# Performance work log

Measured on AMD Instinct MI355X. Metric: run time of the kernel, lower is better.

The kernel has to match this reference:

```python
import jax, jax.numpy as jnp
import numpy as np
from jax import lax

DN = ('NHWC', 'HWIO', 'NHWC')

def _conv(x, k, b, stride=1):
    return lax.conv_general_dilated(x, k, (stride, stride), 'SAME', dimension_numbers=DN) + b

def _tconv(x, k, b):
    return lax.conv_transpose(x, k, (2, 2), 'SAME', dimension_numbers=DN) + b


def setup_inputs() -> dict:
    key = jax.random.key(0)
    ks = jax.random.split(key, 32)
    ki = iter(ks)
    def w(shape, scale=0.05):
        return (jax.random.normal(next(ki), shape, dtype=jnp.float32) * scale)
    inp = {}
    inp['x'] = jax.random.uniform(next(ki), (8, 128, 128, 3), dtype=jnp.float32)
    # encoder
    inp['k1'],  inp['b1']  = w((11, 11, 3, 32)),   jnp.zeros((32,), jnp.float32)
    inp['k1c'], inp['b1c'] = w((3, 3, 32, 32)),    jnp.zeros((32,), jnp.float32)
    inp['k2'],  inp['b2']  = w((11, 11, 32, 64)),  jnp.zeros((64,), jnp.float32)
    inp['k2c'], inp['b2c'] = w((3, 3, 64, 64)),    jnp.zeros((64,), jnp.float32)
    inp['k3'],  inp['b3']  = w((11, 11, 64, 128)), jnp.zeros((128,), jnp.float32)
    inp['k3c'], inp['b3c'] = w((3, 3, 128, 128)),  jnp.zeros((128,), jnp.float32)
    # codebook (codebookSize=256, latent dim 128)
    inp['codebook'] = w((256, 128), 0.1)
    # decoder
    inp['tk1'],  inp['tb1']  = w((5, 5, 128, 64)), jnp.zeros((64,), jnp.float32)
    inp['tk1c'], inp['tb1c'] = w((3, 3, 64, 64)),  jnp.zeros((64,), jnp.float32)
    inp['tk2'],  inp['tb2']  = w((5, 5, 64, 32)),  jnp.zeros((32,), jnp.float32)
    inp['tk2c'], inp['tb2c'] = w((3, 3, 32, 32)),  jnp.zeros((32,), jnp.float32)
    inp['tk3'],  inp['tb3']  = w((5, 5, 32, 32)),  jnp.zeros((32,), jnp.float32)
    inp['tk3c'], inp['tb3c'] = w((3, 3, 32, 3)),   jnp.zeros((3,), jnp.float32)
    return inp


def reference(x, k1, b1, k1c, b1c, k2, b2, k2c, b2c, k3, b3, k3c, b3c,
              codebook, tk1, tb1, tk1c, tb1c, tk2, tb2, tk2c, tb2c,
              tk3, tb3, tk3c, tb3c):
    act = jax.nn.silu  # flax.nnx.swish
    # encoder
    d1 = act(_conv(x, k1, b1, 2))
    d1 = act(_conv(d1, k1c, b1c, 1))
    d2 = act(_conv(d1, k2, b2, 2))
    d2 = act(_conv(d2, k2c, b2c, 1))
    d3 = act(_conv(d2, k3, b3, 2))
    d3 = _conv(d3, k3c, b3c, 1)               # [B, H/8, W/8, 128]
    # vector quantization: squared L2 to each codebook entry
    lat = d3.reshape(-1, 1, 128)              # [N, 1, 128]
    eu_dis = jnp.sum((lat - codebook[None]) ** 2, axis=-1)   # [N, 256]
    idx = jnp.argmin(eu_dis, axis=-1)         # [N]
    quantized = jnp.take(codebook, idx, axis=0).reshape(d3.shape)
    # straight-through estimator
    replaced = lax.stop_gradient(quantized - d3) + d3
    # decoder
    d4 = act(_tconv(replaced, tk1, tb1))
    d4 = act(_conv(d4, tk1c, tb1c, 1))
    d5 = act(_tconv(d4, tk2, tb2))
    d5 = act(_conv(d5, tk2c, tb2c, 1))
    d6 = act(_tconv(d5, tk3, tb3))
    out = _conv(d6, tk3c, tb3c, 1)            # [B, H, W, 3]
    return out
```

## Files before the change

kernel.cpp:

```cpp
#include <hip/hip_runtime.h>

#define DI __device__ __forceinline__
DI float silu_f(float x){ return x * (1.0f/(1.0f+__expf(-x))); }

template<int X> struct LOG2 { static constexpr int v = 1 + LOG2<X/2>::v; };
template<> struct LOG2<1> { static constexpr int v = 0; };

template<int KH,int KW,int STRIDE,int PAD,int CIN,int COUT,int NPIX,
         bool ACT,bool BIAS,int G,int CS,int TOW>
__global__ __launch_bounds__(256) void conv_k(
    const float* __restrict__ in, const float* __restrict__ w,
    const float* __restrict__ bias, float* __restrict__ out,
    int N,int H,int W,int OH,int OW)
{
  constexpr int CLEN = CIN/G;
  constexpr int COB  = COUT/CS;
  constexpr int COQ  = COB/4;
  constexpr int GSH  = LOG2<G>::v;
  constexpr int CSH  = LOG2<CS>::v;
  constexpr int TAPF = CLEN*COB;
  constexpr bool SALL = (KH*KW*TAPF*4) <= 47*1024;
  constexpr int NTAP = SALL ? KH*KW : KW;
  static_assert(CLEN==3 || (CLEN%4)==0, "ci");
  __shared__ float sw[NTAP*TAPF];
  constexpr int SPAN = (TOW>0) ? (TOW-1)*STRIDE + KW : 1;
  constexpr int ROWS = (TOW>0) ? ((256/COQ)*NPIX)/TOW : 1;
  constexpr int CQ4  = (TOW>0 && CLEN!=3) ? CLEN/4 : 1;
  constexpr int SI_F = (TOW==0) ? 1 : (CLEN==3 ? ROWS*SPAN*3 : ROWS*CQ4*SPAN*4);
  __shared__ float si[SI_F];
  static_assert(TOW==0 || NPIX<=2, "tow npix");
  static_assert(TOW==0 || ((256/COQ)*NPIX) % TOW == 0, "rows");

  const int g  = blockIdx.x & (G-1);
  const int cs = (blockIdx.x >> GSH) & (CS-1);
  const int bx = blockIdx.x >> (GSH+CSH);
  const int total = N*OH*OW;
  if (G>1) out += (size_t)g * total * COUT;
  const int ci_off  = g*CLEN;
  const int co_base = cs*COB;

  int idx = bx*256 + (int)threadIdx.x;
  int cq = idx % COQ;
  int pg = idx / COQ;
  int co = cq*4;
  int gco = co_base + co;
  int p0 = pg*NPIX;

  float acc[NPIX][4] = {};
  int iy0[NPIX], ix0[NPIX]; const float* base[NPIX]; bool pv[NPIX];
#pragma unroll
  for (int t=0;t<NPIX;t++){
    int p=p0+t; pv[t]=(p<total); int pp=pv[t]?p:0;
    int ox=pp%OW; int r=pp/OW; int oy=r%OH; int n=r/OH;
    iy0[t]=oy*STRIDE-PAD; ix0[t]=ox*STRIDE-PAD;
    base[t]=in+(size_t)n*H*W*CIN + ci_off;
  }

  auto stage = [&](int tap0){
    constexpr int TQ = TAPF/4;
    constexpr int V  = NTAP*TQ;
    for (int v=threadIdx.x; v<V; v+=256){
      int tap = v / TQ; int rem = v - tap*TQ;
      float4 q;
      if constexpr (CS==1){
        const float4* src = (const float4*)(w + ((size_t)(tap0+tap)*CIN + ci_off)*COUT);
        q = src[rem];
      } else if constexpr (CLEN==3){
        int ci = rem / (COB/4); int r2 = rem - ci*(COB/4);
        q = *(const float4*)(w + ((size_t)(tap0+tap)*CIN + ci)*COUT
                               + co_base + r2*4);
      } else {
        int ci = rem / (COB/4); int r2 = rem - ci*(COB/4);
        q = *(const float4*)(w + ((size_t)(tap0+tap)*CIN + ci_off + ci)*COUT
                               + co_base + r2*4);
      }
      *(float4*)(sw + (size_t)tap*TAPF + rem*4) = q;
    }
  };

  if constexpr (SALL){
    stage(0);
    __syncthreads();
  }

  if constexpr (TOW>0){
    const int pb0 = bx * ((256/COQ)*NPIX);
    const int r0  = pb0 / TOW;
    const int oy0 = r0 % OH;
    const int n0  = r0 / OH;
    int myrow[NPIX], oxl[NPIX];
#pragma unroll
    for (int t=0;t<NPIX;t++){
      int pl = p0 + t - pb0;
      myrow[t] = pl / TOW;
      oxl[t]   = pl - myrow[t]*TOW;
    }

    for (int ky=0; ky<KH; ky++){
      __syncthreads();
      if constexpr (!SALL) stage(ky*KW);
      if constexpr (CLEN==3){
        constexpr int INS = ROWS*SPAN;
        for (int v=(int)threadIdx.x; v<INS; v+=256){
          int r  = v / SPAN;
          int ixo= v - r*SPAN;
          int iy = (oy0+r)*STRIDE - PAD + ky;
          int ix = ixo - PAD;
          bool ok = iy>=0 && iy<H && ix>=0 && ix<W;
          const float* ip = in + ((size_t)(n0*H+iy)*W + ix)*CIN;
          si[v*3+0] = ok?ip[0]:0.f;
          si[v*3+1] = ok?ip[1]:0.f;
          si[v*3+2] = ok?ip[2]:0.f;
        }
      } else {
        constexpr int INQ = ROWS*CQ4*SPAN;
        for (int v=(int)threadIdx.x; v<INQ; v+=256){
          int r  = v / (CQ4*SPAN);
          int rm = v - r*(CQ4*SPAN);
          int q  = rm / SPAN;
          int ixo= rm - q*SPAN;
          int iy = (oy0+r)*STRIDE - PAD + ky;
          int ix = ixo - PAD;
          bool ok = iy>=0 && iy<H && ix>=0 && ix<W;
          float4 val = ok ? *(const float4*)(in + ((size_t)(n0*H+iy)*W + ix)*CIN + ci_off + q*4)
                          : make_float4(0.f,0.f,0.f,0.f);
          *(float4*)&si[(size_t)v*4] = val;
        }
      }
      __syncthreads();
      const float* swr = SALL ? sw + (size_t)ky*KW*TAPF : sw;
      for (int kx=0; kx<KW; kx++){
        const float* swt = swr + (size_t)kx*TAPF;
        if constexpr (CLEN==3){
          float wv[3][4];
          *(float4*)wv[0]=*(const float4*)(swt + 0*COB + co);
          *(float4*)wv[1]=*(const float4*)(swt + 1*COB + co);
          *(float4*)wv[2]=*(const float4*)(swt + 2*COB + co);
#pragma unroll
          for (int t=0;t<NPIX;t++){
            const float* sp = &si[(size_t)(myrow[t]*SPAN + oxl[t]*STRIDE + kx)*3];
            float v0=sp[0], v1=sp[1], v2=sp[2];
#pragma unroll
            for (int j=0;j<4;j++)
              acc[t][j]=fmaf(v0,wv[0][j],fmaf(v1,wv[1][j],fmaf(v2,wv[2][j],acc[t][j])));
          }
        } else {
#pragma unroll 2
          for (int c=0; c<CQ4; c++){
            float wv[4][4];
#pragma unroll
            for (int r=0;r<4;r++)
              *(float4*)wv[r] = *(const float4*)(swt + (c*4+r)*COB + co);
#pragma unroll
            for (int t=0;t<NPIX;t++){
              float va[4];
              *(float4*)va = *(const float4*)&si[(size_t)((myrow[t]*CQ4 + c)*SPAN + oxl[t]*STRIDE + kx)*4];
#pragma unroll
              for (int r=0;r<4;r++)
#pragma unroll
                for (int j=0;j<4;j++)
                  acc[t][j]=fmaf(va[r],wv[r][j],acc[t][j]);
            }
          }
        }
      }
    }
  } else {
    for (int ky=0; ky<KH; ky++){
      if constexpr (!SALL){
        __syncthreads();
        stage(ky*KW);
        __syncthreads();
      }
      const float* swr = SALL ? sw + (size_t)ky*KW*TAPF : sw;
      for (int kx=0; kx<KW; kx++){
        const float* swt = swr + (size_t)kx*TAPF;
        const float* ip[NPIX]; bool ok[NPIX];
#pragma unroll
        for (int t=0;t<NPIX;t++){
          int iy=iy0[t]+ky, ix=ix0[t]+kx;
          ok[t]=pv[t] && iy>=0 && iy<H && ix>=0 && ix<W;
          ip[t]=base[t]+(size_t)(iy*W+ix)*CIN;
        }
        if constexpr (CLEN==3){
          float wv[3][4];
          *(float4*)wv[0]=*(const float4*)(swt + 0*COB + co);
          *(float4*)wv[1]=*(const float4*)(swt + 1*COB + co);
          *(float4*)wv[2]=*(const float4*)(swt + 2*COB + co);
#pragma unroll
          for (int t=0;t<NPIX;t++){
            float v0=ok[t]?ip[t][0]:0.f;
            float v1=ok[t]?ip[t][1]:0.f;
            float v2=ok[t]?ip[t][2]:0.f;
#pragma unroll
            for (int j=0;j<4;j++)
              acc[t][j]=fmaf(v0,wv[0][j],fmaf(v1,wv[1][j],fmaf(v2,wv[2][j],acc[t][j])));
          }
        } else {
#pragma unroll 2
          for (int ci=0; ci<CLEN; ci+=4){
            float wv[4][4];
#pragma unroll
            for (int r=0;r<4;r++)
              *(float4*)wv[r] = *(const float4*)(swt + (ci+r)*COB + co);
#pragma unroll
            for (int t=0;t<NPIX;t++){
              float va[4];
              *(float4*)va = ok[t] ? *(const float4*)(ip[t]+ci)
                                   : make_float4(0.f,0.f,0.f,0.f);
#pragma unroll
              for (int r=0;r<4;r++)
#pragma unroll
                for (int j=0;j<4;j++)
                  acc[t][j]=fmaf(va[r],wv[r][j],acc[t][j]);
            }
          }
        }
      }
    }
  }

  float bv[4]={0.f,0.f,0.f,0.f};
  if constexpr (BIAS) *(float4*)bv = *(const float4*)(bias+gco);
#pragma unroll
  for (int t=0;t<NPIX;t++) if (pv[t]){
    float o[4];
#pragma unroll
    for (int j=0;j<4;j++){
      float v = acc[t][j]+bv[j];
      o[j] = ACT ? silu_f(v) : v;
    }
    *(float4*)(out + (size_t)(p0+t)*COUT + gco) = *(float4*)o;
  }
}

template<int G,int COUT,bool ACT>
__global__ __launch_bounds__(256) void reduce_k(
    const float* __restrict__ p, const float* __restrict__ bias,
    float* __restrict__ out, int n)
{
  int i = (blockIdx.x*256+threadIdx.x)*4;
  if (i>=n) return;
  float a[4]; *(float4*)a = *(const float4*)(p+i);
#pragma unroll
  for (int g=1; g<G; g++){
    float b[4]; *(float4*)b = *(const float4*)(p+(size_t)g*n+i);
#pragma unroll
    for (int j=0;j<4;j++) a[j]+=b[j];
  }
  float bv[4]; *(float4*)bv = *(const float4*)(bias + (i % COUT));
#pragma unroll
  for (int j=0;j<4;j++){
    float v=a[j]+bv[j];
    a[j] = ACT ? silu_f(v) : v;
  }
  *(float4*)(out+i) = *(float4*)a;
}

template<int CIN,int COUT,int NPIX,int G,bool DIRECT>
__global__ __launch_bounds__(256) void tconv_k(
    const float* __restrict__ in, const float* __restrict__ w,
    const float* __restrict__ bias, float* __restrict__ out,
    int N,int H,int W,int OH,int OW)
{
  constexpr int COQ  = COUT/4;
  constexpr int CLEN = CIN/G;
  constexpr int GSH  = LOG2<G>::v;
  constexpr int TAPF = CLEN*COUT;
  __shared__ float sw[TAPF];
  const int par = blockIdx.x & 3;
  const int py = par>>1, px = par&1;
  const int g  = (blockIdx.x>>2) & (G-1);
  const int bx = blockIdx.x >> (2+GSH);
  const int NKY = py?3:2, NKX = px?3:2;
  const int OHh=OH>>1, OWh=OW>>1;
  const int total = N*OHh*OWh;
  if (G>1) out += (size_t)g * N*OH*OW*COUT;

  int idx = bx*256 + (int)threadIdx.x;
  int cq = idx % COQ;
  int pg = idx / COQ;
  int co = cq*4;
  int p0 = pg*NPIX;

  float acc[NPIX][4] = {};
  int yy[NPIX], xx[NPIX], nn[NPIX]; const float* base[NPIX]; bool pv[NPIX];
#pragma unroll
  for (int t=0;t<NPIX;t++){
    int p=p0+t; pv[t]=(p<total); int pp=pv[t]?p:0;
    xx[t]=pp%OWh; int r=pp/OWh; yy[t]=r%OHh; nn[t]=r/OHh;
    base[t]=in+(size_t)nn[t]*H*W*CIN + g*CLEN;
  }

  for (int j=0;j<NKY;j++){
    int ky = 2*j + (py?0:1);
    for (int i=0;i<NKX;i++){
      int kx = 2*i + (px?0:1);
      __syncthreads();
      {
        constexpr int V = TAPF/4;
        const float4* src = (const float4*)(w + ((size_t)(ky*5+kx)*CIN + g*CLEN)*COUT);
        for (int v=threadIdx.x; v<V; v+=256) ((float4*)sw)[v]=src[v];
      }
      __syncthreads();
      const float* ip[NPIX]; bool ok[NPIX];
#pragma unroll
      for (int t=0;t<NPIX;t++){
        int iy=yy[t]+j-1, ix=xx[t]+i-1;
        ok[t]=pv[t] && iy>=0 && iy<H && ix>=0 && ix<W;
        ip[t]=base[t]+(size_t)(iy*W+ix)*CIN;
      }
#pragma unroll 2
      for (int ci=0; ci<CLEN; ci+=4){
        float wv[4][4];
#pragma unroll
        for (int r=0;r<4;r++)
          *(float4*)wv[r] = *(const float4*)(sw + (ci+r)*COUT + co);
#pragma unroll
        for (int t=0;t<NPIX;t++){
          float va[4];
          *(float4*)va = ok[t] ? *(const float4*)(ip[t]+ci)
                               : make_float4(0.f,0.f,0.f,0.f);
#pragma unroll
          for (int r=0;r<4;r++)
#pragma unroll
            for (int jj=0;jj<4;jj++)
              acc[t][jj]=fmaf(va[r],wv[r][jj],acc[t][jj]);
        }
      }
    }
  }

  float bv[4]={0.f,0.f,0.f,0.f};
  if constexpr (DIRECT) *(float4*)bv = *(const float4*)(bias+co);
#pragma unroll
  for (int t=0;t<NPIX;t++) if (pv[t]){
    float o[4];
#pragma unroll
    for (int jj=0;jj<4;jj++){
      float v = acc[t][jj]+bv[jj];
      o[jj] = DIRECT ? silu_f(v) : v;
    }
    *(float4*)(out + (((size_t)nn[t]*OH + (2*yy[t]+py))*OW + (2*xx[t]+px))*COUT + co) = *(float4*)o;
  }
}

__global__ __launch_bounds__(256) void vq_k(
    const float* __restrict__ p, const float* __restrict__ bias,
    const float* __restrict__ cb, float* __restrict__ q, int NLat)
{
  __shared__ float slat[4][128];
  int wave = threadIdx.x >> 6;
  int lane = threadIdx.x & 63;
  int l = blockIdx.x*4 + wave;
  if (l >= NLat) return;
  const float* p0 = p + (size_t)l*128;
  const float* p1 = p0 + (size_t)NLat*128;
  slat[wave][lane]    = p0[lane]    + p1[lane]    + bias[lane];
  slat[wave][lane+64] = p0[lane+64] + p1[lane+64] + bias[lane+64];

  float bestd = INFINITY; int besti = 0;
  for (int c0=0;c0<256;c0+=64){
    int c = c0 + lane;
    const float* cp = cb + (size_t)c*128;
    float d = 0.f;
#pragma unroll 8
    for (int k=0;k<128;k+=4){
      float4 cv = *reinterpret_cast<const float4*>(cp+k);
      float d0 = slat[wave][k+0]-cv.x;
      float d1 = slat[wave][k+1]-cv.y;
      float d2 = slat[wave][k+2]-cv.z;
      float d3 = slat[wave][k+3]-cv.w;
      d += d0*d0; d += d1*d1; d += d2*d2; d += d3*d3;
    }
    if (d < bestd) { bestd = d; besti = c; }
  }
  for (int off=32; off; off>>=1){
    float od = __shfl_down(bestd, off);
    int   oi = __shfl_down(besti, off);
    if (od < bestd || (od == bestd && oi < besti)) { bestd=od; besti=oi; }
  }
  besti = __shfl(besti, 0);
  const float* cp = cb + (size_t)besti*128;
  float* qp = q + (size_t)l*128;
  qp[lane]    = cp[lane];
  qp[lane+64] = cp[lane+64];
}

__global__ __launch_bounds__(256) void conv_last_k(
    const float* __restrict__ in, const float* __restrict__ w,
    float* __restrict__ p, int N,int H,int W)
{
  int g = blockIdx.x % 3;
  int bx = blockIdx.x / 3;
  int pix = bx*256 + threadIdx.x;
  int total = N*H*W;
  if (pix>=total) return;
  int x = pix % W; int r = pix / W; int y = r % H; int n = r / H;
  float a0=0.f, a1=0.f, a2=0.f;
  int iy = y + g - 1;
  if (iy>=0 && iy<H){
    const float* base = in + ((size_t)n*H + iy)*W*32;
    for (int kx=0;kx<3;kx++){
      int ix=x+kx-1; if(ix<0||ix>=W) continue;
      const float* ip = base + (size_t)ix*32;
      const float* wp = w + (size_t)((g*3+kx)*32)*3;
#pragma unroll
      for (int ci=0;ci<32;ci+=4){
        float va[4]; *(float4*)va = *(const float4*)(ip+ci);
        float wv[12];
        *(float4*)(wv+0) = *(const float4*)(wp+ci*3+0);
        *(float4*)(wv+4) = *(const float4*)(wp+ci*3+4);
        *(float4*)(wv+8) = *(const float4*)(wp+ci*3+8);
#pragma unroll
        for (int r2=0;r2<4;r2++){
          a0 = fmaf(va[r2], wv[r2*3+0], a0);
          a1 = fmaf(va[r2], wv[r2*3+1], a1);
          a2 = fmaf(va[r2], wv[r2*3+2], a2);
        }
      }
    }
  }
  float* pp = p + (size_t)g*total*3 + (size_t)pix*3;
  pp[0]=a0; pp[1]=a1; pp[2]=a2;
}

__global__ __launch_bounds__(256) void reduce_last_k(
    const float* __restrict__ p, const float* __restrict__ bias,
    float* __restrict__ out, int n)
{
  int i = (blockIdx.x*256+threadIdx.x)*4;
  if (i>=n) return;
  float a[4]; *(float4*)a = *(const float4*)(p+i);
#pragma unroll
  for (int g=1; g<3; g++){
    float b[4]; *(float4*)b = *(const float4*)(p+(size_t)g*n+i);
#pragma unroll
    for (int j=0;j<4;j++) a[j]+=b[j];
  }
  float o[4];
#pragma unroll
  for (int j=0;j<4;j++) o[j] = a[j] + bias[(i+j)%3];
  *(float4*)(out+i) = *(float4*)o;
}

extern "C" void kernel_launch(void* const* d_in, const int* in_sizes, int n_in,
                              void* d_out, int out_size, void* d_ws, size_t ws_size,
                              hipStream_t stream) {
  const float* x    = (const float*)d_in[0];
  const float* k1   = (const float*)d_in[1];  const float* b1  = (const float*)d_in[2];
  const float* k1c  = (const float*)d_in[3];  const float* b1c = (const float*)d_in[4];
  const float* k2   = (const float*)d_in[5];  const float* b2  = (const float*)d_in[6];
  const float* k2c  = (const float*)d_in[7];  const float* b2c = (const float*)d_in[8];
  const float* k3   = (const float*)d_in[9];  const float* b3  = (const float*)d_in[10];
  const float* k3c  = (const float*)d_in[11]; const float* b3c = (const float*)d_in[12];
  const float* cb   = (const float*)d_in[13];
  const float* tk1  = (const float*)d_in[14]; const float* tb1  = (const float*)d_in[15];
  const float* tk1c = (const float*)d_in[16]; const float* tb1c = (const float*)d_in[17];
  const float* tk2  = (const float*)d_in[18]; const float* tb2  = (const float*)d_in[19];
  const float* tk2c = (const float*)d_in[20]; const float* tb2c = (const float*)d_in[21];
  const float* tk3  = (const float*)d_in[22]; const float* tb3  = (const float*)d_in[23];
  const float* tk3c = (const float*)d_in[24]; const float* tb3c = (const float*)d_in[25];
  float* out = (float*)d_out;

  float* S  = (float*)d_ws;
  float* W0 = S;
  float* W1 = S + 1048576;
  float* P  = S + 2097152;
  dim3 blk(256);

  conv_k<11,11,2,4,  3, 32,2,true ,true ,1,2,64><<< 512,blk,0,stream>>>(x,  k1,  b1,  W0, 8,128,128,64,64);
  conv_k< 3, 3,1,1, 32, 32,2,true ,true ,1,2,64><<< 512,blk,0,stream>>>(W0, k1c, b1c, W1, 8,64,64,64,64);
  conv_k<11,11,2,4, 32, 64,2,false,false,2,2,32><<< 512,blk,0,stream>>>(W1, k2,  nullptr, P, 8,64,64,32,32);
  reduce_k<2, 64,true><<< 512,blk,0,stream>>>(P, b2,  W0, 524288);
  conv_k< 3, 3,1,1, 64, 64,1,true ,true ,1,2,32><<< 512,blk,0,stream>>>(W0, k2c, b2c, W1, 8,32,32,32,32);
  conv_k<11,11,2,4, 64,128,2,false,false,4,4,16><<< 512,blk,0,stream>>>(W1, k3,  nullptr, P, 8,32,32,16,16);
  reduce_k<4,128,true><<< 256,blk,0,stream>>>(P, b3,  W0, 262144);
  conv_k< 3, 3,1,1,128,128,1,false,false,2,4,16><<< 512,blk,0,stream>>>(W0, k3c, nullptr, P, 8,16,16,16,16);
  vq_k<<<512,blk,0,stream>>>(P, b3c, cb, W1, 2048);
  tconv_k<128,64,1,4,false><<<2048,blk,0,stream>>>(W1, tk1, nullptr, P, 8,16,16,32,32);
  reduce_k<4, 64,true><<< 512,blk,0,stream>>>(P, tb1,  W0, 524288);
  conv_k< 3, 3,1,1, 64, 64,2,false,false,2,4,32><<< 512,blk,0,stream>>>(W0, tk1c, nullptr, P, 8,32,32,32,32);
  reduce_k<2, 64,true><<< 512,blk,0,stream>>>(P, tb1c, W1, 524288);
  tconv_k< 64,32,1,2,false><<<2048,blk,0,stream>>>(W1, tk2, nullptr, P, 8,32,32,64,64);
  reduce_k<2, 32,true><<<1024,blk,0,stream>>>(P, tb2,  W0, 1048576);
  conv_k< 3, 3,1,1, 32, 32,2,true ,true ,1,2,64><<< 512,blk,0,stream>>>(W0, tk2c, tb2c, W1, 8,64,64,64,64);
  tconv_k< 32,32,2,1,true ><<<2048,blk,0,stream>>>(W1, tk3, tb3, P, 8,64,64,128,128);
  conv_last_k<<<1536,blk,0,stream>>>(P, tk3c, S, 8,128,128);
  reduce_last_k<<<384,blk,0,stream>>>(S, tb3c, out, 393216);
}
```

Measured before the change: 462.7 us.

## Stage input row tiles and all tap weights in shared memory for transposed convs

Replaces the transposed-conv kernel with a row-blocked version that loads all parity taps' weights once and a haloed tile of input rows into shared memory, removing the per-tap syncthreads and redundant global input reads. Adds an output-channel split (CS) and changes launch configurations for the three decoder upsampling layers. This costs more shared memory per block, which may reduce occupancy, and requires blocks to cover whole rows.

```diff
diff --git a/kernel.cpp b/kernel.cpp
--- a/kernel.cpp
+++ b/kernel.cpp
@@ -257,70 +257,100 @@
   *(float4*)(out+i) = *(float4*)a;
 }
 
-template<int CIN,int COUT,int NPIX,int G,bool DIRECT>
-__global__ __launch_bounds__(256) void tconv_k(
+template<int CIN,int COUT,int NPIX,int G,int CS,int IW,bool DIRECT>
+__global__ __launch_bounds__(256) void tconv_rb(
     const float* __restrict__ in, const float* __restrict__ w,
     const float* __restrict__ bias, float* __restrict__ out,
     int N,int H,int W,int OH,int OW)
 {
-  constexpr int COQ  = COUT/4;
   constexpr int CLEN = CIN/G;
+  constexpr int COB  = COUT/CS;
+  constexpr int COQ  = COB/4;
   constexpr int GSH  = LOG2<G>::v;
-  constexpr int TAPF = CLEN*COUT;
-  __shared__ float sw[TAPF];
+  constexpr int CSH  = LOG2<CS>::v;
+  constexpr int TAPF = CLEN*COB;
+  constexpr int PPB  = (256/COQ)*NPIX;
+  static_assert(PPB % IW == 0, "whole rows");
+  constexpr int ROWS_O = PPB/IW;
+  constexpr int NRI  = ROWS_O + 2;
+  constexpr int SPAN = IW + 2;
+  constexpr int CQ4  = CLEN/4;
+  __shared__ float sw[9*TAPF];
+  __shared__ float si[NRI*CQ4*SPAN*4];
+
   const int par = blockIdx.x & 3;
   const int py = par>>1, px = par&1;
   const int g  = (blockIdx.x>>2) & (G-1);
-  const int bx = blockIdx.x >> (2+GSH);
+  const int cs = (blockIdx.x>>(2+GSH)) & (CS-1);
+  const int bx = blockIdx.x >> (2+GSH+CSH);
   const int NKY = py?3:2, NKX = px?3:2;
-  const int OHh=OH>>1, OWh=OW>>1;
-  const int total = N*OHh*OWh;
-  if (G>1) out += (size_t)g * N*OH*OW*COUT;
-
-  int idx = bx*256 + (int)threadIdx.x;
+  const int OHh = OH>>1;
+  if (G>1) out += (size_t)g * (size_t)N*OH*OW*COUT;
+  const int co_base = cs*COB;
+
+  const int tid = (int)threadIdx.x;
+  int idx = bx*256 + tid;
   int cq = idx % COQ;
   int pg = idx / COQ;
   int co = cq*4;
   int p0 = pg*NPIX;
+  const int pb0 = bx*PPB;
+  const int R0  = pb0 / IW;
+  const int oy0 = R0 % OHh;
+  const int n0  = R0 / OHh;
+
+  int myrow[NPIX], xx[NPIX];
+#pragma unroll
+  for (int t=0;t<NPIX;t++){
+    int lp = p0 + t - pb0;
+    myrow[t] = lp / IW;
+    xx[t]    = lp - myrow[t]*IW;
+  }
+
+  {
+    constexpr int TQ = TAPF/4;
+    const int V = NKY*NKX*TQ;
+    for (int v=tid; v<V; v+=256){
+      int tap = v / TQ; int rem = v - tap*TQ;
+      int j = tap / NKX, i = tap - j*NKX;
+      int ky = 2*j + (py?0:1), kx = 2*i + (px?0:1);
+      int ci = rem / (COB/4); int r2 = rem - ci*(COB/4);
+      float4 q = *(const float4*)(w + ((size_t)(ky*5+kx)*CIN + g*CLEN + ci)*COUT
+                                    + co_base + r2*4);
+      *(float4*)(sw + (size_t)(j*3+i)*TAPF + rem*4) = q;
+    }
+  }
+  {
+    constexpr int INQ = NRI*CQ4*SPAN;
+    for (int v=tid; v<INQ; v+=256){
+      int r  = v / (CQ4*SPAN);
+      int rm = v - r*(CQ4*SPAN);
+      int q  = rm / SPAN;
+      int cc = rm - q*SPAN;
+      int iy = oy0 - 1 + r;
+      int ix = cc - 1;
+      bool ok = iy>=0 && iy<H && ix>=0 && ix<W;
+      float4 val = ok ? *(const float4*)(in + ((size_t)(n0*H+iy)*W + ix)*CIN + g*CLEN + q*4)
+                      : make_float4(0.f,0.f,0.f,0.f);
+      *(float4*)&si[(size_t)v*4] = val;
+    }
+  }
+  __syncthreads();
 
   float acc[NPIX][4] = {};
-  int yy[NPIX], xx[NPIX], nn[NPIX]; const float* base[NPIX]; bool pv[NPIX];
-#pragma unroll
-  for (int t=0;t<NPIX;t++){
-    int p=p0+t; pv[t]=(p<total); int pp=pv[t]?p:0;
-    xx[t]=pp%OWh; int r=pp/OWh; yy[t]=r%OHh; nn[t]=r/OHh;
-    base[t]=in+(size_t)nn[t]*H*W*CIN + g*CLEN;
-  }
-
   for (int j=0;j<NKY;j++){
-    int ky = 2*j + (py?0:1);
     for (int i=0;i<NKX;i++){
-      int kx = 2*i + (px?0:1);
-      __syncthreads();
-      {
-        constexpr int V = TAPF/4;
-        const float4* src = (const float4*)(w + ((size_t)(ky*5+kx)*CIN + g*CLEN)*COUT);
-        for (int v=threadIdx.x; v<V; v+=256) ((float4*)sw)[v]=src[v];
-      }
-      __syncthreads();
-      const float* ip[NPIX]; bool ok[NPIX];
-#pragma unroll
-      for (int t=0;t<NPIX;t++){
-        int iy=yy[t]+j-1, ix=xx[t]+i-1;
-        ok[t]=pv[t] && iy>=0 && iy<H && ix>=0 && ix<W;
-        ip[t]=base[t]+(size_t)(iy*W+ix)*CIN;
-      }
+      const float* swt = sw + (size_t)(j*3+i)*TAPF;
 #pragma unroll 2
-      for (int ci=0; ci<CLEN; ci+=4){
+      for (int c=0;c<CQ4;c++){
         float wv[4][4];
 #pragma unroll
         for (int r=0;r<4;r++)
-          *(float4*)wv[r] = *(const float4*)(sw + (ci+r)*COUT + co);
+          *(float4*)wv[r] = *(const float4*)(swt + (c*4+r)*COB + co);
 #pragma unroll
         for (int t=0;t<NPIX;t++){
           float va[4];
-          *(float4*)va = ok[t] ? *(const float4*)(ip[t]+ci)
-                               : make_float4(0.f,0.f,0.f,0.f);
+          *(float4*)va = *(const float4*)&si[(size_t)(((myrow[t]+j)*CQ4 + c)*SPAN + (xx[t]+i))*4];
 #pragma unroll
           for (int r=0;r<4;r++)
 #pragma unroll
@@ -332,16 +362,16 @@
   }
 
   float bv[4]={0.f,0.f,0.f,0.f};
-  if constexpr (DIRECT) *(float4*)bv = *(const float4*)(bias+co);
-#pragma unroll
-  for (int t=0;t<NPIX;t++) if (pv[t]){
+  if constexpr (DIRECT) *(float4*)bv = *(const float4*)(bias+co_base+co);
+#pragma unroll
+  for (int t=0;t<NPIX;t++){
     float o[4];
 #pragma unroll
     for (int jj=0;jj<4;jj++){
       float v = acc[t][jj]+bv[jj];
       o[jj] = DIRECT ? silu_f(v) : v;
     }
-    *(float4*)(out + (((size_t)nn[t]*OH + (2*yy[t]+py))*OW + (2*xx[t]+px))*COUT + co) = *(float4*)o;
+    *(float4*)(out + (((size_t)n0*OH + (2*(oy0+myrow[t])+py))*OW + (2*xx[t]+px))*COUT + co_base+co) = *(float4*)o;
   }
 }
 
@@ -478,14 +508,14 @@
   reduce_k<4,128,true><<< 256,blk,0,stream>>>(P, b3,  W0, 262144);
   conv_k< 3, 3,1,1,128,128,1,false,false,2,4,16><<< 512,blk,0,stream>>>(W0, k3c, nullptr, P, 8,16,16,16,16);
   vq_k<<<512,blk,0,stream>>>(P, b3c, cb, W1, 2048);
-  tconv_k<128,64,1,4,false><<<2048,blk,0,stream>>>(W1, tk1, nullptr, P, 8,16,16,32,32);
+  tconv_rb<128,64,1,4,2,16,false><<<2048,blk,0,stream>>>(W1, tk1, nullptr, P, 8,16,16,32,32);
   reduce_k<4, 64,true><<< 512,blk,0,stream>>>(P, tb1,  W0, 524288);
   conv_k< 3, 3,1,1, 64, 64,2,false,false,2,4,32><<< 512,blk,0,stream>>>(W0, tk1c, nullptr, P, 8,32,32,32,32);
   reduce_k<2, 64,true><<< 512,blk,0,stream>>>(P, tb1c, W1, 524288);
-  tconv_k< 64,32,1,2,false><<<2048,blk,0,stream>>>(W1, tk2, nullptr, P, 8,32,32,64,64);
+  tconv_rb< 64,32,1,2,1,32,false><<<2048,blk,0,stream>>>(W1, tk2, nullptr, P, 8,32,32,64,64);
   reduce_k<2, 32,true><<<1024,blk,0,stream>>>(P, tb2,  W0, 1048576);
   conv_k< 3, 3,1,1, 32, 32,2,true ,true ,1,2,64><<< 512,blk,0,stream>>>(W0, tk2c, tb2c, W1, 8,64,64,64,64);
-  tconv_k< 32,32,2,1,true ><<<2048,blk,0,stream>>>(W1, tk3, tb3, P, 8,64,64,128,128);
+  tconv_rb< 32,32,1,1,2,64,true ><<<4096,blk,0,stream>>>(W1, tk3, tb3, P, 8,64,64,128,128);
   conv_last_k<<<1536,blk,0,stream>>>(P, tk3c, S, 8,128,128);
   reduce_last_k<<<384,blk,0,stream>>>(S, tb3c, out, 393216);
 }
```

New measurement: 450.5 us. -2.6%, faster.
